# Performance work log

Measured on AMD Instinct MI355X. Metric: run time of the kernel, lower is better.

The kernel has to match this reference:

```python
import jax, jax.numpy as jnp
import numpy as np
from jax import lax

B, C, H, W = 8, 512, 64, 64
KD, VD, S = 64, 256, 2
EPS = 1e-5

def conv2d(x, w, stride=1, pad=0):
    return lax.conv_general_dilated(x, w, (stride, stride), [(pad, pad), (pad, pad)],
                                    dimension_numbers=('NCHW', 'OIHW', 'NCHW'))

def conv_transpose2d(x, w, stride=2, pad=1, out_pad=1):
    # torch ConvTranspose2d weight layout: (in, out, kh, kw) -> flip spatial, swap in/out
    k = w.shape[2]
    w_t = jnp.transpose(w[:, :, ::-1, ::-1], (1, 0, 2, 3))  # (out, in, kh, kw)
    p_lo = k - 1 - pad
    p_hi = k - 1 - pad + out_pad
    return lax.conv_general_dilated(x, w_t, (1, 1), [(p_lo, p_hi), (p_lo, p_hi)],
                                    lhs_dilation=(stride, stride),
                                    dimension_numbers=('NCHW', 'OIHW', 'NCHW'))

def batch_norm(x, scale, bias, mean, var):
    inv = scale / jnp.sqrt(var + EPS)
    return x * inv[None, :, None, None] + (bias - mean * inv)[None, :, None, None]

def setup_inputs() -> dict:
    key = jax.random.key(0)
    ks = jax.random.split(key, 20)
    f = lambda i, shape, sc=0.05: jax.random.normal(ks[i], shape, dtype=jnp.float32) * sc
    inp = {
        'x': jax.random.normal(ks[0], (B, C, H, W), dtype=jnp.float32),
        'w_q': f(1, (KD, C, 1, 1)), 'b_q': f(2, (KD,)),
        'bn_q_s': 1.0 + f(3, (KD,)), 'bn_q_b': f(4, (KD,)),
        'bn_q_m': f(5, (KD,)), 'bn_q_v': 1.0 + 0.1 * jax.random.uniform(ks[6], (KD,), dtype=jnp.float32),
        'w_k': f(7, (KD, C, 3, 3)), 'b_k': f(8, (KD,)),
        'bn_k_s': 1.0 + f(9, (KD,)), 'bn_k_b': f(10, (KD,)),
        'bn_k_m': f(11, (KD,)), 'bn_k_v': 1.0 + 0.1 * jax.random.uniform(ks[12], (KD,), dtype=jnp.float32),
        'w_v': f(13, (VD, C, 1, 1)), 'b_v': f(14, (VD,)),
        'w_d': f(15, (VD, C, 3, 3)),
        'bn_d_s': 1.0 + f(16, (C,)), 'bn_d_b': f(17, (C,)),
        'bn_d_m': f(18, (C,)), 'bn_d_v': 1.0 + 0.1 * jax.random.uniform(ks[19], (C,), dtype=jnp.float32),
    }
    return inp

def reference(x, w_q, b_q, bn_q_s, bn_q_b, bn_q_m, bn_q_v,
              w_k, b_k, bn_k_s, bn_k_b, bn_k_m, bn_k_v,
              w_v, b_v, w_d, bn_d_s, bn_d_b, bn_d_m, bn_d_v):
    b, c, h, w = x.shape
    n = h * w
    hk, wk_ = h // S, w // S
    nk = hk * wk_
    # query: 1x1 conv + BN -> [b, KD, n]
    q = batch_norm(conv2d(x, w_q) + b_q[None, :, None, None], bn_q_s, bn_q_b, bn_q_m, bn_q_v)
    q = q.reshape(b, KD, n)
    # key: 3x3 strided conv + BN -> [b, nk, KD]
    k = batch_norm(conv2d(x, w_k, stride=S, pad=1) + b_k[None, :, None, None], bn_k_s, bn_k_b, bn_k_m, bn_k_v)
    k = k.reshape(b, KD, nk)
    # energy: [b, nk, n]; softmax over n
    energy = jnp.einsum('bdm,bdn->bmn', k, q)
    attention = jax.nn.softmax(energy, axis=-1)
    # value: [b, VD, n]
    v = (conv2d(x, w_v) + b_v[None, :, None, None]).reshape(b, VD, n)
    # out: [b, VD, nk]
    out = jnp.einsum('bvn,bmn->bvm', v, attention)
    out = out.reshape(b, VD, hk, wk_)
    out = jax.nn.relu(batch_norm(conv_transpose2d(out, w_d), bn_d_s, bn_d_b, bn_d_m, bn_d_v))
    return out + x
```

## Files before the change

### kernel.cpp

```cpp
#include <hip/hip_runtime.h>
#include <hip/hip_bf16.h>
#include <cstdint>

#define BN_EPS 1e-5f

typedef short bf16x8 __attribute__((ext_vector_type(8)));
typedef _Float16 f16x8 __attribute__((ext_vector_type(8)));
typedef float f32x4 __attribute__((ext_vector_type(4)));

__device__ __forceinline__ float bf16hi_to_f(uint32_t hi) {
    union { uint32_t u; float f; } c; c.u = hi; return c.f;
}
__device__ __forceinline__ uint32_t f_to_bf16(float f) {
    union { float f; uint32_t u; } c; c.f = f;
    uint32_t r = c.u + 0x7fffu + ((c.u >> 16) & 1u);
    return r >> 16;
}
__device__ __forceinline__ unsigned short f_to_f16(float f) {
    _Float16 h = (_Float16)f;
    union { _Float16 h; unsigned short u; } c; c.h = h; return c.u;
}

__global__ __launch_bounds__(256) void pam_prep1(
    const float* __restrict__ wk, const float* __restrict__ wq, const float* __restrict__ wv,
    const float* __restrict__ bq, const float* __restrict__ qs, const float* __restrict__ qb,
    const float* __restrict__ qm, const float* __restrict__ qv,
    const float* __restrict__ bk, const float* __restrict__ ks, const float* __restrict__ kb,
    const float* __restrict__ km, const float* __restrict__ kv,
    const float* __restrict__ ds, const float* __restrict__ db,
    const float* __restrict__ dm, const float* __restrict__ dv,
    unsigned short* __restrict__ wkF, unsigned short* __restrict__ wqvF,
    float* __restrict__ affQ, float* __restrict__ affK, float* __restrict__ affD) {
    int blk = blockIdx.x, t = threadIdx.x;
    if (blk < 1152) {
        int o = blk * 256 + t;
        int c = o & 511; int d = (o >> 9) & 63; int tap = o >> 15;
        float v = wk[((size_t)d * 512 + c) * 9 + tap];
        int dt = d >> 4, lm = d & 15, cs = c >> 5, g = (c >> 3) & 3, j = c & 7;
        size_t idx = (((size_t)((tap * 4 + dt) * 16 + cs)) * 64 + g * 16 + lm) * 8 + j;
        wkF[idx] = f_to_f16(v);
    } else if (blk < 1792) {
        int o = (blk - 1152) * 256 + t;
        int c = o & 511, R = o >> 9;
        float v;
        if (R < 64) {
            float inv = qs[R] * rsqrtf(qv[R] + BN_EPS);
            v = wq[(size_t)R * 512 + c] * inv;
        } else {
            v = wv[(size_t)(R - 64) * 512 + c];
        }
        int ct = R >> 4, lmr = R & 15, cs = c >> 5, g = (c >> 3) & 3, j = c & 7;
        size_t idx = (((size_t)(ct * 16 + cs)) * 64 + g * 16 + lmr) * 8 + j;
        wqvF[idx] = f_to_f16(v);
    } else {
        int i = (blk - 1792) * 256 + t;
        if (i < 64) {
            float inv = qs[i] * rsqrtf(qv[i] + BN_EPS);
            affQ[i] = inv; affQ[64 + i] = bq[i] * inv + qb[i] - qm[i] * inv;
        } else if (i < 128) {
            int k = i - 64;
            float inv = ks[k] * rsqrtf(kv[k] + BN_EPS);
            affK[k] = inv; affK[64 + k] = bk[k] * inv + kb[k] - km[k] * inv;
        } else if (i < 640) {
            int k = i - 128;
            float inv = ds[k] * rsqrtf(dv[k] + BN_EPS);
            affD[k] = inv; affD[512 + k] = db[k] - dm[k] * inv;
        }
    }
}

__global__ __launch_bounds__(256) void pam_prep2(
    const float* __restrict__ wd, unsigned short* __restrict__ wdF,
    unsigned short* __restrict__ p) {
    int blk = blockIdx.x, t = threadIdx.x;
    if (blk < 4608) {
        int o = blk * 256 + t;
        int ci = o & 255; int co = (o >> 8) & 511; int tap = o >> 17;
        float v = wd[(size_t)ci * 4608 + co * 9 + tap];
        int ct = co >> 4, lmr = co & 15, cs = ci >> 5, g = (ci >> 3) & 3, j = ci & 7;
        size_t idx = (((size_t)(tap * 32 + ct) * 8 + cs) * 512) + g * 128 + lmr * 8 + j;
        wdF[idx] = (unsigned short)f_to_bf16(v);
    } else {
        size_t i = ((size_t)(blk - 4608) * 256 + t) * 8;
        uint4 z = make_uint4(0, 0, 0, 0);
        *(uint4*)(p + i) = z;
    }
}

__global__ __launch_bounds__(256) void pam_xt(const float* __restrict__ x,
                                              unsigned short* __restrict__ xF) {
    __shared__ unsigned short lds[2][32][72];
    int t = threadIdx.x;
    int ri = blockIdx.x;
    int b = blockIdx.y;
    size_t rowbase = ((size_t)b * 65 + ri) * 65 * 512;
    uint4 z = make_uint4(0, 0, 0, 0);
    if (ri == 0) {
        for (int idx = t; idx < 65 * 512 / 8; idx += 256)
            *(uint4*)(xF + rowbase + (size_t)idx * 8) = z;
        return;
    }
    if (t < 64)
        *(uint4*)(xF + rowbase + (size_t)t * 8) = z;
    int hi = ri - 1;
    int wi = t & 63, cl = t >> 6;
    int px = t >> 2, c4 = (t & 3) * 8;
    const float* xb = x + (size_t)b * 512 * 4096 + (size_t)hi * 64 + wi;
    for (int ch = 0; ch < 16; ++ch) {
        unsigned short v[8];
        #pragma unroll
        for (int j = 0; j < 8; j++)
            v[j] = f_to_f16(xb[(size_t)(ch * 32 + cl * 8 + j) * 4096]);
        #pragma unroll
        for (int j = 0; j < 8; j++)
            lds[ch & 1][cl * 8 + j][wi] = v[j];
        __syncthreads();
        unsigned short w[8];
        #pragma unroll
        for (int j = 0; j < 8; j++)
            w[j] = lds[ch & 1][c4 + j][px];
        uint4 pw = make_uint4((uint32_t)w[0] | ((uint32_t)w[1] << 16),
                              (uint32_t)w[2] | ((uint32_t)w[3] << 16),
                              (uint32_t)w[4] | ((uint32_t)w[5] << 16),
                              (uint32_t)w[6] | ((uint32_t)w[7] << 16));
        *(uint4*)(xF + rowbase + (size_t)(px + 1) * 512 + ch * 32 + c4) = pw;
    }
}

__global__ __launch_bounds__(256, 4) void pam_qv_mfma(
    const unsigned short* __restrict__ xF,
    const unsigned short* __restrict__ wqvF,
    const float* __restrict__ affQ, const float* __restrict__ bv,
    unsigned short* __restrict__ qF,
    unsigned short* __restrict__ vF) {
    int t = threadIdx.x;
    int hb = blockIdx.x, b = blockIdx.y;
    int h = hb >> 1, phf = hb & 1;
    int wv_ = t >> 6, lane = t & 63, g = lane >> 4, lm = lane & 15;
    int ct0 = wv_ * 5;

    f32x4 acc[5][2];
    #pragma unroll
    for (int m = 0; m < 5; m++)
        #pragma unroll
        for (int n = 0; n < 2; n++) acc[m][n] = (f32x4){0.f, 0.f, 0.f, 0.f};

    const unsigned short* xb = xF + (((size_t)(b * 65) + h + 1) * 65 + 1) * 512
                               + (size_t)(phf * 32 + lm) * 512 + g * 8;
    const unsigned short* wb = wqvF + (size_t)lane * 8;

    #pragma unroll 4
    for (int cs = 0; cs < 16; cs++) {
        int coff = cs * 32;
        f16x8 bfr[2];
        #pragma unroll
        for (int nt = 0; nt < 2; nt++)
            bfr[nt] = *(const f16x8*)(xb + (size_t)nt * 16 * 512 + coff);
        f16x8 afr[5];
        #pragma unroll
        for (int m = 0; m < 5; m++)
            afr[m] = *(const f16x8*)(wb + (size_t)((ct0 + m) * 16 + cs) * 512);
        #pragma unroll
        for (int m = 0; m < 5; m++)
            #pragma unroll
            for (int n = 0; n < 2; n++)
                acc[m][n] = __builtin_amdgcn_mfma_f32_16x16x32_f16(afr[m], bfr[n], acc[m][n], 0, 0, 0);
    }

    #pragma unroll
    for (int m = 0; m < 5; m++) {
        #pragma unroll
        for (int i = 0; i < 4; i++) {
            int R = (ct0 + m) * 16 + g * 4 + i;
            float shift = (R < 64) ? affQ[64 + R] : bv[R - 64];
            if (R < 64) {
                int s_ = R >> 5, gF = (R >> 3) & 3, jF = R & 7;
                #pragma unroll
                for (int nt = 0; nt < 2; nt++) {
                    int p = h * 64 + phf * 32 + nt * 16 + lm;
                    float val = acc[m][nt][i] + shift;
                    size_t idx = (size_t)(b * 256 + (p >> 4)) * 1024 + s_ * 512 + gF * 128 + (p & 15) * 8 + jF;
                    qF[idx] = f_to_f16(val);
                }
            } else {
                int c = R - 64;
                #pragma unroll
                for (int nt = 0; nt < 2; nt++) {
                    int p = h * 64 + phf * 32 + nt * 16 + lm;
                    float val = acc[m][nt][i] + shift;
                    size_t idx = (size_t)(b * 128 + (p >> 5)) * 8192 + (c >> 4) * 512 +
                                 ((p >> 3) & 3) * 128 + (c & 15) * 8 + (p & 7);
                    vF[idx] = (unsigned short)f_to_bf16(val);
                }
            }
        }
    }
}

__global__ __launch_bounds__(1024, 4) void pam_kconv_mfma(
    const unsigned short* __restrict__ xF,
    const unsigned short* __restrict__ wkF,
    const float* __restrict__ affK,
    unsigned short* __restrict__ kF) {
    __shared__ float red[3 * 4 * 64 * 8];
    int t = threadIdx.x;
    int hk = blockIdx.x, b = blockIdx.y;
    int wid = t >> 6, lane = t & 63, g = lane >> 4, lm = lane & 15;
    int dt = wid & 3, cq = wid >> 2;
    int goff = g * 8;
    f32x4 acc0 = (f32x4){0.f, 0.f, 0.f, 0.f};
    f32x4 acc1 = (f32x4){0.f, 0.f, 0.f, 0.f};
    #pragma unroll
    for (int r = 0; r < 3; r++) {
        size_t arow = ((size_t)(b * 65 + 2 * hk + r)) * 65 * 512;
        #pragma unroll
        for (int s = 0; s < 3; s++) {
            size_t aoff = arow + (size_t)(2 * lm + s) * 512 + goff;
            const unsigned short* pa0 = xF + aoff;
            int tap = r * 3 + s;
            const unsigned short* pb = wkF + (((size_t)(tap * 4 + dt) * 16) * 64 + lane) * 8;
            #pragma unroll
            for (int k = 0; k < 4; k++) {
                int c0 = cq * 128 + k * 32;
                f16x8 a0 = *(const f16x8*)(pa0 + c0);
                f16x8 a1 = *(const f16x8*)(pa0 + 32 * 512 + c0);
                f16x8 bf = *(const f16x8*)(pb + (size_t)(c0 >> 5) * 512);
                acc0 = __builtin_amdgcn_mfma_f32_16x16x32_f16(a0, bf, acc0, 0, 0, 0);
                acc1 = __builtin_amdgcn_mfma_f32_16x16x32_f16(a1, bf, acc1, 0, 0, 0);
            }
        }
    }
    if (cq > 0) {
        float* dst = red + (((size_t)(cq - 1) * 4 + dt) * 64 + lane) * 8;
        *(f32x4*)dst = acc0;
        *(f32x4*)(dst + 4) = acc1;
    }
    __syncthreads();
    if (cq != 0) return;
    #pragma unroll
    for (int q = 0; q < 3; q++) {
        const float* src = red + (((size_t)q * 4 + dt) * 64 + lane) * 8;
        f32x4 p0 = *(const f32x4*)src;
        f32x4 p1 = *(const f32x4*)(src + 4);
        acc0 += p0; acc1 += p1;
    }
    int d = dt * 16 + lm;
    float sc = affK[d], sh = affK[64 + d];
    int s_ = d >> 5, gF = (d >> 3) & 3, jF = d & 7;
    #pragma unroll
    for (int i = 0; i < 4; i++) {
        int m1 = hk * 32 + g * 4 + i;
        int m2 = m1 + 16;
        float v0 = fmaf(acc0[i], sc, sh);
        float v1 = fmaf(acc1[i], sc, sh);
        size_t i1 = (size_t)(b * 64 + (m1 >> 4)) * 1024 + s_ * 512 + gF * 128 + (m1 & 15) * 8 + jF;
        kF[i1] = f_to_f16(v0);
        size_t i2 = (size_t)(b * 64 + (m2 >> 4)) * 1024 + s_ * 512 + gF * 128 + (m2 & 15) * 8 + jF;
        kF[i2] = f_to_f16(v1);
    }
}

__global__ __launch_bounds__(512, 4) void pam_attn(
    const unsigned short* __restrict__ qF,
    const unsigned short* __restrict__ kF,
    const unsigned short* __restrict__ vF, unsigned short* __restrict__ outsP) {
    __shared__ unsigned short Pl[16384];
    __shared__ float redM[8][16];
    __shared__ float redS[8][16];
    int t = threadIdx.x;
    int b = blockIdx.x, mt = blockIdx.y;
    int wid = t >> 6, lane = t & 63;
    int g = lane >> 4, lm = lane & 15;

    size_t kidx = (size_t)(b * 64 + mt) * 1024 + g * 128 + lm * 8;
    f16x8 kf0 = *(const f16x8*)(kF + kidx);
    f16x8 kf1 = *(const f16x8*)(kF + kidx + 512);

    float Mrun[4], rsum[4];
    #pragma unroll
    for (int i = 0; i < 4; i++) { Mrun[i] = -3e38f; rsum[i] = 0.f; }
    f32x4 oA0 = (f32x4){0.f,0.f,0.f,0.f}, oA1 = oA0, oB0 = oA0, oB1 = oA0;

    const unsigned short* qhb = qF + (size_t)(b * 256) * 1024 + g * 128 + lm * 8;
    const unsigned short* vb  = vF + (size_t)b * 1048576 + (wid * 2) * 512 + g * 128 + lm * 8;

    for (int ph = 0; ph < 4; ++ph) {
        f32x4 ev[8];
        #pragma unroll
        for (int f = 0; f < 8; f++) ev[f] = (f32x4){0.f, 0.f, 0.f, 0.f};
        int ft0 = ph * 64 + wid * 8;
        #pragma unroll
        for (int f = 0; f < 8; f++) {
            const unsigned short* qhp = qhb + (size_t)(ft0 + f) * 1024;
            f16x8 qf0 = *(const f16x8*)(qhp);
            f16x8 qf1 = *(const f16x8*)(qhp + 512);
            f32x4 e = ev[f];
            e = __builtin_amdgcn_mfma_f32_16x16x32_f16(kf0, qf0, e, 0, 0, 0);
            e = __builtin_amdgcn_mfma_f32_16x16x32_f16(kf1, qf1, e, 0, 0, 0);
            ev[f] = e;
        }
        float pm[4];
        #pragma unroll
        for (int i = 0; i < 4; i++) {
            float m_ = ev[0][i];
            #pragma unroll
            for (int f = 1; f < 8; f++) m_ = fmaxf(m_, ev[f][i]);
            #pragma unroll
            for (int off = 1; off < 16; off <<= 1) m_ = fmaxf(m_, __shfl_xor(m_, off));
            pm[i] = m_;
        }
        if (lm == 0) {
            #pragma unroll
            for (int i = 0; i < 4; i++) redM[wid][g * 4 + i] = pm[i];
        }
        __syncthreads();
        float rfac[4];
        #pragma unroll
        for (int i = 0; i < 4; i++) {
            float pmax = redM[0][g * 4 + i];
            #pragma unroll
            for (int w2 = 1; w2 < 8; w2++) pmax = fmaxf(pmax, redM[w2][g * 4 + i]);
            float Mn = fmaxf(Mrun[i], pmax);
            rfac[i] = __expf(Mrun[i] - Mn);
            Mrun[i] = Mn;
        }
        #pragma unroll
        for (int i = 0; i < 4; i++) {
            rsum[i] *= rfac[i];
            oA0[i] *= rfac[i]; oA1[i] *= rfac[i];
            oB0[i] *= rfac[i]; oB1[i] *= rfac[i];
        }
        #pragma unroll
        for (int f = 0; f < 8; f++) {
            int ntl = wid * 8 + f;
            int ks = ntl >> 1;
            int gF = (ntl & 1) * 2 + (lm >> 3);
            int jF = lm & 7;
            #pragma unroll
            for (int i = 0; i < 4; i++) {
                float p = __expf(ev[f][i] - Mrun[i]);
                uint32_t u = f_to_bf16(p);
                rsum[i] += bf16hi_to_f(u << 16);
                Pl[((ks * 4 + gF) * 16 + (g * 4 + i)) * 8 + jF] = (unsigned short)u;
            }
        }
        __syncthreads();
        #pragma unroll 8
        for (int ks = 0; ks < 32; ks++) {
            bf16x8 pa = *(const bf16x8*)(Pl + ((ks * 4 + g) * 16 + lm) * 8);
            bf16x8 bvA = *(const bf16x8*)(vb + (size_t)(ph * 32 + ks) * 8192);
            bf16x8 bvB = *(const bf16x8*)(vb + (size_t)(ph * 32 + ks) * 8192 + 512);
            if (ks & 1) {
                oA1 = __builtin_amdgcn_mfma_f32_16x16x32_bf16(pa, bvA, oA1, 0, 0, 0);
                oB1 = __builtin_amdgcn_mfma_f32_16x16x32_bf16(pa, bvB, oB1, 0, 0, 0);
            } else {
                oA0 = __builtin_amdgcn_mfma_f32_16x16x32_bf16(pa, bvA, oA0, 0, 0, 0);
                oB0 = __builtin_amdgcn_mfma_f32_16x16x32_bf16(pa, bvB, oB0, 0, 0, 0);
            }
        }
    }

    #pragma unroll
    for (int i = 0; i < 4; i++) {
        float s_ = rsum[i];
        #pragma unroll
        for (int off = 1; off < 16; off <<= 1) s_ += __shfl_xor(s_, off);
        rsum[i] = s_;
    }
    __syncthreads();
    if (lm == 0) {
        #pragma unroll
        for (int i = 0; i < 4; i++) redS[wid][g * 4 + i] = rsum[i];
    }
    __syncthreads();
    f32x4 ofA = oA0 + oA1;
    f32x4 ofB = oB0 + oB1;
    int c0 = wid * 32;
    #pragma unroll
    for (int i = 0; i < 4; i++) {
        float s_ = 0.f;
        #pragma unroll
        for (int w2 = 0; w2 < 8; w2++) s_ += redS[w2][g * 4 + i];
        float sinv = 1.f / s_;
        int m = mt * 16 + g * 4 + i;
        int hk2 = m >> 5, wk2 = m & 31;
        unsigned short* op = outsP + (((size_t)(b * 33 + hk2)) * 33 + wk2) * 256;
        op[c0 + lm]      = (unsigned short)f_to_bf16(ofA[i] * sinv);
        op[c0 + 16 + lm] = (unsigned short)f_to_bf16(ofB[i] * sinv);
    }
}

template<int LROW, int KH, int KW>
__device__ __forceinline__ void deconv_tap(
    const unsigned short* __restrict__ wdF,
    const char* lb, int ct0, int lane, int lm, f32x4 (&acc)[2][2][2]) {
    constexpr int wop = (KW == 1) ? 0 : 1;
    constexpr int dw = (KW == 0) ? 1 : 0;
    constexpr int tap = KH * 3 + KW;
    int g = lane >> 4;
    int p0 = LROW * 33 + lm + dw;
    int p1 = p0 + 16;
    uint32_t s0 = ((uint32_t)(p0 & 7)) << 4;
    uint32_t s1 = ((uint32_t)(p1 & 7)) << 4;
    uint32_t b0a = (uint32_t)p0 * 512 + (uint32_t)g * 16;
    uint32_t b1a = (uint32_t)p1 * 512 + (uint32_t)g * 16;
    const unsigned short* a0p = wdF + ((size_t)(tap * 32 + ct0) * 8) * 512 + lane * 8;
    const unsigned short* a1p = a0p + 8 * 512;
    #pragma unroll
    for (int cs = 0; cs < 8; cs++) {
        bf16x8 bv0 = *(const bf16x8*)(lb + ((b0a + (uint32_t)cs * 64) ^ s0));
        bf16x8 bv1 = *(const bf16x8*)(lb + ((b1a + (uint32_t)cs * 64) ^ s1));
        bf16x8 a0 = *(const bf16x8*)(a0p + cs * 512);
        bf16x8 a1 = *(const bf16x8*)(a1p + cs * 512);
        acc[wop][0][0] = __builtin_amdgcn_mfma_f32_16x16x32_bf16(a0, bv0, acc[wop][0][0], 0, 0, 0);
        acc[wop][0][1] = __builtin_amdgcn_mfma_f32_16x16x32_bf16(a0, bv1, acc[wop][0][1], 0, 0, 0);
        acc[wop][1][0] = __builtin_amdgcn_mfma_f32_16x16x32_bf16(a1, bv0, acc[wop][1][0], 0, 0, 0);
        acc[wop][1][1] = __builtin_amdgcn_mfma_f32_16x16x32_bf16(a1, bv1, acc[wop][1][1], 0, 0, 0);
    }
}

__device__ __forceinline__ void deconv_epi(
    const f32x4 (&acc)[2][2][2], const float* __restrict__ affD,
    const float* __restrict__ x, float* __restrict__ out,
    int b, int ho, int co0, int lm, int g) {
    #pragma unroll
    for (int mf = 0; mf < 2; mf++) {
        #pragma unroll
        for (int i = 0; i < 4; i++) {
            int co = co0 + mf * 16 + g * 4 + i;
            float sc = affD[co], sh = affD[512 + co];
            const float* xr = x + (((size_t)b * 512 + co) * 64 + ho) * 64;
            float* orow = out + (((size_t)b * 512 + co) * 64 + ho) * 64;
            #pragma unroll
            for (int nf = 0; nf < 2; nf++) {
                int wp = nf * 16 + lm;
                float2 xv = *(const float2*)(xr + 2 * wp);
                float2 st;
                st.x = fmaxf(fmaf(acc[0][mf][nf][i], sc, sh), 0.f) + xv.x;
                st.y = fmaxf(fmaf(acc[1][mf][nf][i], sc, sh), 0.f) + xv.y;
                *(float2*)(orow + 2 * wp) = st;
            }
        }
    }
}

__global__ __launch_bounds__(512, 4) void pam_deconv_mfma(
    const unsigned short* __restrict__ outsP,
    const unsigned short* __restrict__ wdF,
    const float* __restrict__ affD, const float* __restrict__ x, float* __restrict__ out) {
    __shared__ unsigned short Pb[16896];
    int t = threadIdx.x;
    int h0 = blockIdx.x, b = blockIdx.y, zh = blockIdx.z;
    const unsigned short* src = outsP + ((size_t)(b * 33 + h0) * 33) * 256;
    for (int idx = t; idx < 2112; idx += 512) {
        uint4 v = *(const uint4*)(src + (size_t)idx * 8);
        uint32_t byte = (uint32_t)idx * 16;
        byte ^= ((byte >> 9) & 7) << 4;
        *(uint4*)((char*)Pb + byte) = v;
    }
    __syncthreads();

    int wid = t >> 6, lane = t & 63, g = lane >> 4, lm = lane & 15;
    int ct0 = (zh * 8 + wid) * 2, co0 = (zh * 8 + wid) * 32;
    const char* lb = (const char*)Pb;

    {
        f32x4 acc[2][2][2];
        #pragma unroll
        for (int a = 0; a < 2; a++)
            #pragma unroll
            for (int m = 0; m < 2; m++)
                #pragma unroll
                for (int n = 0; n < 2; n++) acc[a][m][n] = (f32x4){0.f, 0.f, 0.f, 0.f};
        deconv_tap<0, 1, 0>(wdF, lb, ct0, lane, lm, acc);
        deconv_tap<0, 1, 1>(wdF, lb, ct0, lane, lm, acc);
        deconv_tap<0, 1, 2>(wdF, lb, ct0, lane, lm, acc);
        deconv_epi(acc, affD, x, out, b, 2 * h0, co0, lm, g);
    }
    {
        f32x4 acc[2][2][2];
        #pragma unroll
        for (int a = 0; a < 2; a++)
            #pragma unroll
            for (int m = 0; m < 2; m++)
                #pragma unroll
                for (int n = 0; n < 2; n++) acc[a][m][n] = (f32x4){0.f, 0.f, 0.f, 0.f};
        deconv_tap<0, 2, 0>(wdF, lb, ct0, lane, lm, acc);
        deconv_tap<0, 2, 1>(wdF, lb, ct0, lane, lm, acc);
        deconv_tap<0, 2, 2>(wdF, lb, ct0, lane, lm, acc);
        deconv_tap<1, 0, 0>(wdF, lb, ct0, lane, lm, acc);
        deconv_tap<1, 0, 1>(wdF, lb, ct0, lane, lm, acc);
        deconv_tap<1, 0, 2>(wdF, lb, ct0, lane, lm, acc);
        deconv_epi(acc, affD, x, out, b, 2 * h0 + 1, co0, lm, g);
    }
}

extern "C" void kernel_launch(void* const* d_in, const int* in_sizes, int n_in,
                              void* d_out, int out_size, void* d_ws, size_t ws_size,
                              hipStream_t stream) {
    const float* x   = (const float*)d_in[0];
    const float* w_q = (const float*)d_in[1];
    const float* b_q = (const float*)d_in[2];
    const float* qs  = (const float*)d_in[3];
    const float* qb  = (const float*)d_in[4];
    const float* qm  = (const float*)d_in[5];
    const float* qv  = (const float*)d_in[6];
    const float* w_k = (const float*)d_in[7];
    const float* b_k = (const float*)d_in[8];
    const float* ks  = (const float*)d_in[9];
    const float* kb  = (const float*)d_in[10];
    const float* km  = (const float*)d_in[11];
    const float* kv  = (const float*)d_in[12];
    const float* w_v = (const float*)d_in[13];
    const float* b_v = (const float*)d_in[14];
    const float* w_d = (const float*)d_in[15];
    const float* ds  = (const float*)d_in[16];
    const float* db  = (const float*)d_in[17];
    const float* dm  = (const float*)d_in[18];
    const float* dv  = (const float*)d_in[19];
    float* out = (float*)d_out;

    char* wsb = (char*)d_ws;
    unsigned short* qF    = (unsigned short*)(wsb);
    unsigned short* vF    = (unsigned short*)(wsb + 8388608);
    unsigned short* kF    = (unsigned short*)(wsb + 25165824);
    unsigned short* wqvF  = (unsigned short*)(wsb + 26214400);
    unsigned short* wkF   = (unsigned short*)(wsb + 27262976);
    float*          affQ  = (float*)(wsb + 28442624);
    float*          affK  = (float*)(wsb + 28443136);
    float*          affD  = (float*)(wsb + 28443648);
    unsigned short* xF    = (unsigned short*)(wsb + 28447744);
    unsigned short* outsP = (unsigned short*)(wsb + 28447744);
    unsigned short* wdF   = (unsigned short*)(wsb + 32908288);

    hipLaunchKernelGGL(pam_prep1, dim3(1795), dim3(256), 0, stream,
                       w_k, w_q, w_v, b_q, qs, qb, qm, qv, b_k, ks, kb, km, kv,
                       ds, db, dm, dv, wkF, wqvF, affQ, affK, affD);
    hipLaunchKernelGGL(pam_xt, dim3(65, 8), dim3(256), 0, stream, x, xF);
    hipLaunchKernelGGL(pam_qv_mfma, dim3(128, 8), dim3(256), 0, stream,
                       xF, wqvF, affQ, b_v, qF, vF);
    hipLaunchKernelGGL(pam_kconv_mfma, dim3(32, 8), dim3(1024), 0, stream,
                       xF, wkF, affK, kF);
    hipLaunchKernelGGL(pam_prep2, dim3(5697), dim3(256), 0, stream, w_d, wdF, outsP);
    hipLaunchKernelGGL(pam_attn, dim3(8, 64), dim3(512), 0, stream,
                       qF, kF, vF, outsP);
    hipLaunchKernelGGL(pam_deconv_mfma, dim3(32, 8, 2), dim3(512), 0, stream,
                       outsP, wdF, affD, x, out);
}
```

Before: 224.2 us.

## Process two query-row tiles per attention block to halve V reloads

Each attention workgroup now handles 32 key rows (two 16-row tiles) instead of 16, with waves split between the two tiles for the energy/softmax phase and all waves sharing each V fragment across both tiles in the PV MFMA loop. This halves the grid and the number of times V is streamed from global memory per row, at the cost of twice as many softmax phases per block and more accumulators per wave. The grid drops to 256 blocks, which may underfill the GPU's compute units.

```diff
diff --git a/kernel.cpp b/kernel.cpp
--- a/kernel.cpp
+++ b/kernel.cpp
@@ -265,30 +265,31 @@
     const unsigned short* __restrict__ kF,
     const unsigned short* __restrict__ vF, unsigned short* __restrict__ outsP) {
     __shared__ unsigned short Pl[16384];
-    __shared__ float redM[8][16];
-    __shared__ float redS[8][16];
+    __shared__ float redM[2][4][16];
+    __shared__ float redS[2][4][16];
     int t = threadIdx.x;
-    int b = blockIdx.x, mt = blockIdx.y;
+    int b = blockIdx.x, mt2 = blockIdx.y;
     int wid = t >> 6, lane = t & 63;
     int g = lane >> 4, lm = lane & 15;
-
-    size_t kidx = (size_t)(b * 64 + mt) * 1024 + g * 128 + lm * 8;
+    int mtl = wid & 1, wp = wid >> 1;
+
+    size_t kidx = (size_t)(b * 64 + mt2 * 2 + mtl) * 1024 + g * 128 + lm * 8;
     f16x8 kf0 = *(const f16x8*)(kF + kidx);
     f16x8 kf1 = *(const f16x8*)(kF + kidx + 512);
 
-    float Mrun[4], rsum[4];
-    #pragma unroll
-    for (int i = 0; i < 4; i++) { Mrun[i] = -3e38f; rsum[i] = 0.f; }
-    f32x4 oA0 = (f32x4){0.f,0.f,0.f,0.f}, oA1 = oA0, oB0 = oA0, oB1 = oA0;
+    float Mrun[2][4], rsum[4];
+    #pragma unroll
+    for (int i = 0; i < 4; i++) { Mrun[0][i] = -3e38f; Mrun[1][i] = -3e38f; rsum[i] = 0.f; }
+    f32x4 o0A = (f32x4){0.f,0.f,0.f,0.f}, o0B = o0A, o1A = o0A, o1B = o0A;
 
     const unsigned short* qhb = qF + (size_t)(b * 256) * 1024 + g * 128 + lm * 8;
     const unsigned short* vb  = vF + (size_t)b * 1048576 + (wid * 2) * 512 + g * 128 + lm * 8;
 
-    for (int ph = 0; ph < 4; ++ph) {
+    for (int ph = 0; ph < 8; ++ph) {
         f32x4 ev[8];
         #pragma unroll
         for (int f = 0; f < 8; f++) ev[f] = (f32x4){0.f, 0.f, 0.f, 0.f};
-        int ft0 = ph * 64 + wid * 8;
+        int ft0 = ph * 32 + wp * 8;
         #pragma unroll
         for (int f = 0; f < 8; f++) {
             const unsigned short* qhp = qhb + (size_t)(ft0 + f) * 1024;
@@ -311,52 +312,53 @@
         }
         if (lm == 0) {
             #pragma unroll
-            for (int i = 0; i < 4; i++) redM[wid][g * 4 + i] = pm[i];
+            for (int i = 0; i < 4; i++) redM[mtl][wp][g * 4 + i] = pm[i];
         }
         __syncthreads();
-        float rfac[4];
+        float rfac[2][4];
+        #pragma unroll
+        for (int mt = 0; mt < 2; mt++) {
+            #pragma unroll
+            for (int i = 0; i < 4; i++) {
+                float pmax = redM[mt][0][g * 4 + i];
+                #pragma unroll
+                for (int w2 = 1; w2 < 4; w2++) pmax = fmaxf(pmax, redM[mt][w2][g * 4 + i]);
+                float Mn = fmaxf(Mrun[mt][i], pmax);
+                rfac[mt][i] = __expf(Mrun[mt][i] - Mn);
+                Mrun[mt][i] = Mn;
+            }
+        }
         #pragma unroll
         for (int i = 0; i < 4; i++) {
-            float pmax = redM[0][g * 4 + i];
-            #pragma unroll
-            for (int w2 = 1; w2 < 8; w2++) pmax = fmaxf(pmax, redM[w2][g * 4 + i]);
-            float Mn = fmaxf(Mrun[i], pmax);
-            rfac[i] = __expf(Mrun[i] - Mn);
-            Mrun[i] = Mn;
-        }
-        #pragma unroll
-        for (int i = 0; i < 4; i++) {
-            rsum[i] *= rfac[i];
-            oA0[i] *= rfac[i]; oA1[i] *= rfac[i];
-            oB0[i] *= rfac[i]; oB1[i] *= rfac[i];
+            rsum[i] *= rfac[mtl][i];
+            o0A[i] *= rfac[0][i]; o0B[i] *= rfac[0][i];
+            o1A[i] *= rfac[1][i]; o1B[i] *= rfac[1][i];
         }
         #pragma unroll
         for (int f = 0; f < 8; f++) {
-            int ntl = wid * 8 + f;
+            int ntl = wp * 8 + f;
             int ks = ntl >> 1;
             int gF = (ntl & 1) * 2 + (lm >> 3);
             int jF = lm & 7;
             #pragma unroll
             for (int i = 0; i < 4; i++) {
-                float p = __expf(ev[f][i] - Mrun[i]);
+                float p = __expf(ev[f][i] - Mrun[mtl][i]);
                 uint32_t u = f_to_bf16(p);
                 rsum[i] += bf16hi_to_f(u << 16);
-                Pl[((ks * 4 + gF) * 16 + (g * 4 + i)) * 8 + jF] = (unsigned short)u;
+                Pl[((ks * 4 + gF) * 32 + mtl * 16 + g * 4 + i) * 8 + jF] = (unsigned short)u;
             }
         }
         __syncthreads();
-        #pragma unroll 8
-        for (int ks = 0; ks < 32; ks++) {
-            bf16x8 pa = *(const bf16x8*)(Pl + ((ks * 4 + g) * 16 + lm) * 8);
-            bf16x8 bvA = *(const bf16x8*)(vb + (size_t)(ph * 32 + ks) * 8192);
-            bf16x8 bvB = *(const bf16x8*)(vb + (size_t)(ph * 32 + ks) * 8192 + 512);
-            if (ks & 1) {
-                oA1 = __builtin_amdgcn_mfma_f32_16x16x32_bf16(pa, bvA, oA1, 0, 0, 0);
-                oB1 = __builtin_amdgcn_mfma_f32_16x16x32_bf16(pa, bvB, oB1, 0, 0, 0);
-            } else {
-                oA0 = __builtin_amdgcn_mfma_f32_16x16x32_bf16(pa, bvA, oA0, 0, 0, 0);
-                oB0 = __builtin_amdgcn_mfma_f32_16x16x32_bf16(pa, bvB, oB0, 0, 0, 0);
-            }
+        #pragma unroll 4
+        for (int ks = 0; ks < 16; ks++) {
+            bf16x8 pa0 = *(const bf16x8*)(Pl + ((ks * 4 + g) * 32 + lm) * 8);
+            bf16x8 pa1 = *(const bf16x8*)(Pl + ((ks * 4 + g) * 32 + 16 + lm) * 8);
+            bf16x8 bvA = *(const bf16x8*)(vb + (size_t)(ph * 16 + ks) * 8192);
+            bf16x8 bvB = *(const bf16x8*)(vb + (size_t)(ph * 16 + ks) * 8192 + 512);
+            o0A = __builtin_amdgcn_mfma_f32_16x16x32_bf16(pa0, bvA, o0A, 0, 0, 0);
+            o0B = __builtin_amdgcn_mfma_f32_16x16x32_bf16(pa0, bvB, o0B, 0, 0, 0);
+            o1A = __builtin_amdgcn_mfma_f32_16x16x32_bf16(pa1, bvA, o1A, 0, 0, 0);
+            o1B = __builtin_amdgcn_mfma_f32_16x16x32_bf16(pa1, bvB, o1B, 0, 0, 0);
         }
     }
 
@@ -370,23 +372,26 @@
     __syncthreads();
     if (lm == 0) {
         #pragma unroll
-        for (int i = 0; i < 4; i++) redS[wid][g * 4 + i] = rsum[i];
+        for (int i = 0; i < 4; i++) redS[mtl][wp][g * 4 + i] = rsum[i];
     }
     __syncthreads();
-    f32x4 ofA = oA0 + oA1;
-    f32x4 ofB = oB0 + oB1;
     int c0 = wid * 32;
     #pragma unroll
-    for (int i = 0; i < 4; i++) {
-        float s_ = 0.f;
-        #pragma unroll
-        for (int w2 = 0; w2 < 8; w2++) s_ += redS[w2][g * 4 + i];
-        float sinv = 1.f / s_;
-        int m = mt * 16 + g * 4 + i;
-        int hk2 = m >> 5, wk2 = m & 31;
-        unsigned short* op = outsP + (((size_t)(b * 33 + hk2)) * 33 + wk2) * 256;
-        op[c0 + lm]      = (unsigned short)f_to_bf16(ofA[i] * sinv);
-        op[c0 + 16 + lm] = (unsigned short)f_to_bf16(ofB[i] * sinv);
+    for (int mt = 0; mt < 2; mt++) {
+        #pragma unroll
+        for (int i = 0; i < 4; i++) {
+            float s_ = 0.f;
+            #pragma unroll
+            for (int w2 = 0; w2 < 4; w2++) s_ += redS[mt][w2][g * 4 + i];
+            float sinv = 1.f / s_;
+            int m = mt2 * 32 + mt * 16 + g * 4 + i;
+            int hk2 = m >> 5, wk2 = m & 31;
+            unsigned short* op = outsP + (((size_t)(b * 33 + hk2)) * 33 + wk2) * 256;
+            float vA = (mt == 0) ? o0A[i] : o1A[i];
+            float vB = (mt == 0) ? o0B[i] : o1B[i];
+            op[c0 + lm]      = (unsigned short)f_to_bf16(vA * sinv);
+            op[c0 + 16 + lm] = (unsigned short)f_to_bf16(vB * sinv);
+        }
     }
 }
 
@@ -542,7 +547,7 @@
     hipLaunchKernelGGL(pam_kconv_mfma, dim3(32, 8), dim3(1024), 0, stream,
                        xF, wkF, affK, kF);
     hipLaunchKernelGGL(pam_prep2, dim3(5697), dim3(256), 0, stream, w_d, wdF, outsP);
-    hipLaunchKernelGGL(pam_attn, dim3(8, 64), dim3(512), 0, stream,
+    hipLaunchKernelGGL(pam_attn, dim3(8, 32), dim3(512), 0, stream,
                        qF, kF, vF, outsP);
     hipLaunchKernelGGL(pam_deconv_mfma, dim3(32, 8, 2), dim3(512), 0, stream,
                        outsP, wdF, affD, x, out);
```

Result: slower. 243.5 us (+8.6%).
